# Performance work log

Measured on AMD Instinct MI355X. Metric: run time of the kernel, lower is better.

## Reference

```python
import jax, jax.numpy as jnp
import numpy as np

N_NODES = 10000
N_EDGES = 160000
HID = 256
NBOND = 6
NATOM = 62
NLAYERS = 6


def _lin_init(key, fan_in, fan_out):
    # torch nn.Linear default: U(-1/sqrt(fan_in), 1/sqrt(fan_in))
    kw, kb = jax.random.split(key)
    bound = 1.0 / np.sqrt(fan_in)
    w = jax.random.uniform(kw, (fan_in, fan_out), jnp.float32, -bound, bound)
    b = jax.random.uniform(kb, (fan_out,), jnp.float32, -bound, bound)
    return w, b


def setup_inputs() -> dict:
    key = jax.random.key(0)
    ks = jax.random.split(key, 32)
    atom_features = jax.random.normal(ks[0], (N_NODES, NATOM), jnp.float32)
    edge_index = jax.random.randint(ks[1], (2, N_EDGES), 0, N_NODES, jnp.int64 if jax.config.jax_enable_x64 else jnp.int32)
    edge_features = jax.random.normal(ks[2], (N_EDGES, NBOND), jnp.float32)

    embed_w, embed_b = _lin_init(ks[3], NATOM, HID)

    msg_in = 2 * HID + NBOND  # 518
    mw1, mb1, mw2, mb2 = [], [], [], []
    uw1, ub1, uw2, ub2 = [], [], [], []
    for i in range(NLAYERS):
        k = jax.random.split(ks[4 + i], 4)
        w, b = _lin_init(k[0], msg_in, HID); mw1.append(w); mb1.append(b)
        w, b = _lin_init(k[1], HID, HID); mw2.append(w); mb2.append(b)
        w, b = _lin_init(k[2], 2 * HID, HID); uw1.append(w); ub1.append(b)
        w, b = _lin_init(k[3], HID, HID); uw2.append(w); ub2.append(b)

    r_w1, r_b1 = _lin_init(ks[20], HID, HID)
    r_w2, r_b2 = _lin_init(ks[21], HID, HID // 2)
    r_w3, r_b3 = _lin_init(ks[22], HID // 2, 1)

    return {
        "atom_features": atom_features,
        "edge_index": edge_index,
        "edge_features": edge_features,
        "embed_w": embed_w, "embed_b": embed_b,
        "msg_w1": jnp.stack(mw1), "msg_b1": jnp.stack(mb1),
        "msg_w2": jnp.stack(mw2), "msg_b2": jnp.stack(mb2),
        "upd_w1": jnp.stack(uw1), "upd_b1": jnp.stack(ub1),
        "upd_w2": jnp.stack(uw2), "upd_b2": jnp.stack(ub2),
        "r_w1": r_w1, "r_b1": r_b1,
        "r_w2": r_w2, "r_b2": r_b2,
        "r_w3": r_w3, "r_b3": r_b3,
    }


def _mlp2(x, w1, b1, w2, b2):
    return jnp.maximum(x @ w1 + b1, 0.0) @ w2 + b2


def reference(atom_features, edge_index, edge_features,
              embed_w, embed_b,
              msg_w1, msg_b1, msg_w2, msg_b2,
              upd_w1, upd_b1, upd_w2, upd_b2,
              r_w1, r_b1, r_w2, r_b2, r_w3, r_b3):
    src, dst = edge_index[0], edge_index[1]
    n = atom_features.shape[0]
    x = atom_features @ embed_w + embed_b  # [N, H]
    for l in range(msg_w1.shape[0]):
        # per-edge gather + concat -> message MLP
        msg_in = jnp.concatenate([x[src], x[dst], edge_features], axis=-1)  # [E, 2H+B]
        msgs = _mlp2(msg_in, msg_w1[l], msg_b1[l], msg_w2[l], msg_b2[l])  # [E, H]
        # scatter-add into dst nodes
        agg = jax.ops.segment_sum(msgs, dst, num_segments=n)  # [N, H]
        x = _mlp2(jnp.concatenate([x, agg], axis=-1), upd_w1[l], upd_b1[l], upd_w2[l], upd_b2[l])
    # readout (dropout is identity in eval mode)
    h = jnp.maximum(x @ r_w1 + r_b1, 0.0)
    h = jnp.maximum(h @ r_w2 + r_b2, 0.0)
    out = h @ r_w3 + r_b3  # [N, 1]
    return out.mean(axis=0)  # [1]
```

## Files before the change

### kernel.cpp

```cpp
#include <hip/hip_runtime.h>
#include <hip/hip_bf16.h>
#include <hip/hip_fp16.h>


#define HID 256
#define CAP 128

typedef _Float16 h8 __attribute__((ext_vector_type(8)));
typedef float f32x4 __attribute__((ext_vector_type(4)));

__device__ __forceinline__ void unpack_h8(const int4& r, float* f) {
    const __half2* h = reinterpret_cast<const __half2*>(&r);
#pragma unroll
    for (int k = 0; k < 4; ++k) {
        float2 t = __half22float2(h[k]);
        f[2 * k] = t.x;
        f[2 * k + 1] = t.y;
    }
}

__device__ __forceinline__ void unpack_h4(const int2& r, float* f) {
    const __half2* h = reinterpret_cast<const __half2*>(&r);
    float2 t0 = __half22float2(h[0]);
    float2 t1 = __half22float2(h[1]);
    f[0] = t0.x; f[1] = t0.y; f[2] = t1.x; f[3] = t1.y;
}

__device__ __forceinline__ void gld16(const void* g, void* l) {
    __builtin_amdgcn_global_load_lds(
        (const __attribute__((address_space(1))) void*)g,
        (__attribute__((address_space(3))) void*)l, 16, 0, 0);
}

__device__ __forceinline__ int swz(int row) { return (row + (row >> 2)) & 3; }


struct CDesc {
    const float* src;
    __half* dst;
    int Kreal, Kpad, srcN, tile0, dstStride;
};
struct CTab {
    CDesc d[32];
    int nd;
};

__device__ void convert_body(const CTab& tab, int bid) {
    int idx = 0;
    for (int i = 1; i < tab.nd; ++i)
        if (tab.d[i].tile0 <= bid) idx = i;
    const CDesc d = tab.d[idx];
    const int q = bid - d.tile0;
    const int ntN = d.srcN >> 6;
    const int kb = (q / ntN) * 32;
    const int nb = (q % ntN) * 64;
    const int n = nb + (threadIdx.x & 63);
    const int k0 = kb + (threadIdx.x >> 6) * 8;
    h8 v;
#pragma unroll
    for (int j = 0; j < 8; ++j) {
        int k = k0 + j;
        v[j] = (_Float16)((k < d.Kreal) ? d.src[(size_t)k * d.srcN + n] : 0.f);
    }
    *reinterpret_cast<h8*>(&d.dst[(size_t)n * d.dstStride + k0]) = v;
}


__global__ void conv_kernel(const float* __restrict__ atom,
                            __half* __restrict__ atomH, int NA,
                            int atomB, CTab tab) {
    if ((int)blockIdx.x < atomB) {
        int i = blockIdx.x * blockDim.x + threadIdx.x;
        if (i < NA) {
            int r = i >> 3, seg = i & 7;
            h8 v;
#pragma unroll
            for (int j = 0; j < 8; ++j) {
                int c = seg * 8 + j;
                v[j] = (_Float16)((c < 62) ? atom[(size_t)r * 62 + c] : 0.f);
            }
            *reinterpret_cast<h8*>(&atomH[(size_t)r * 64 + seg * 8]) = v;
        }
    } else {
        convert_body(tab, blockIdx.x - atomB);
    }
}


struct BDesc { float* out; const float* base; const float* v1; const float* B1;
               const float* v2; const float* B2; };
struct BTab { BDesc d[31]; };


#define ASTR 40

struct FDesc { const float* U2; const __half* Wfb; __half* dst; int stride; };
struct FTab { FDesc d[22]; };

__device__ void fold_tile(unsigned char* ldsraw, const FDesc& dd, int t4) {
    _Float16* Ah = (_Float16*)ldsraw;
    _Float16* Bh = (_Float16*)(ldsraw + 64 * ASTR * 2);
    const int rowBase = (t4 >> 2) * 64;
    const int colBase = (t4 & 3) * 64;

    const int tid = threadIdx.x;
    const int lane = tid & 63;
    const int wave = tid >> 6;
    const int waveM = (wave >> 1) * 32;
    const int waveN = (wave & 1) * 32;
    const int m0 = lane & 15;
    const int quad = lane >> 4;
    const int sr = tid >> 2;
    const int sseg = tid & 3;

    const f32x4 z = {0.f, 0.f, 0.f, 0.f};
    f32x4 acc[2][2] = {{z, z}, {z, z}};

    for (int kb = 0; kb < 256; kb += 32) {
        {
            size_t off = (size_t)(rowBase + sr) * 256 + kb + sseg * 8;
            *reinterpret_cast<int4*>(&Ah[sr * ASTR + sseg * 8]) =
                *reinterpret_cast<const int4*>(&dd.Wfb[off]);
        }
        {
            const float* Bp = dd.U2 + (size_t)(colBase + sr) * 256 + kb + sseg * 8;
            float4 u0 = *reinterpret_cast<const float4*>(Bp);
            float4 u1 = *reinterpret_cast<const float4*>(Bp + 4);
            h8 v;
            v[0] = (_Float16)u0.x; v[1] = (_Float16)u0.y;
            v[2] = (_Float16)u0.z; v[3] = (_Float16)u0.w;
            v[4] = (_Float16)u1.x; v[5] = (_Float16)u1.y;
            v[6] = (_Float16)u1.z; v[7] = (_Float16)u1.w;
            *reinterpret_cast<h8*>(&Bh[sr * ASTR + sseg * 8]) = v;
        }
        __syncthreads();

        const h8 a0 = *reinterpret_cast<const h8*>(&Ah[(waveM + m0) * ASTR + quad * 8]);
        const h8 a1 = *reinterpret_cast<const h8*>(&Ah[(waveM + 16 + m0) * ASTR + quad * 8]);
        const h8 b0 = *reinterpret_cast<const h8*>(&Bh[(waveN + m0) * ASTR + quad * 8]);
        const h8 b1 = *reinterpret_cast<const h8*>(&Bh[(waveN + 16 + m0) * ASTR + quad * 8]);

        acc[0][0] = __builtin_amdgcn_mfma_f32_16x16x32_f16(a0, b0, acc[0][0], 0, 0, 0);
        acc[0][1] = __builtin_amdgcn_mfma_f32_16x16x32_f16(a0, b1, acc[0][1], 0, 0, 0);
        acc[1][0] = __builtin_amdgcn_mfma_f32_16x16x32_f16(a1, b0, acc[1][0], 0, 0, 0);
        acc[1][1] = __builtin_amdgcn_mfma_f32_16x16x32_f16(a1, b1, acc[1][1], 0, 0, 0);

        __syncthreads();
    }

#pragma unroll
    for (int tm = 0; tm < 2; ++tm)
#pragma unroll
        for (int reg = 0; reg < 4; ++reg) {
            int n = rowBase + waveM + tm * 16 + quad * 4 + reg;
#pragma unroll
            for (int tn = 0; tn < 2; ++tn) {
                int k = colBase + waveN + tn * 16 + m0;
                dd.dst[(size_t)n * dd.stride + k] = __float2half_rn(acc[tm][tn][reg]);
            }
        }
}


template <int TN>
__device__ void gemm_tile(
    unsigned char* lds, int bx, int by,
    const __half* __restrict__ A, int lda,
    const __half* __restrict__ W, int K,
    const float* __restrict__ bias,
    __half* __restrict__ C, int M, int Nc, int do_relu) {
    constexpr int BUF = 4096 + TN * 2048;

    const int tid = threadIdx.x;
    const int lane = tid & 63;
    const int wave = tid >> 6;
    const int m0 = lane & 15;
    const int quad = lane >> 4;
    const int waveM = (wave >> 1) * 32;
    const int waveN = (wave & 1) * (TN * 16);
    const int rowBase = bx * 64;
    const int colBase = by * (TN * 32);

    const int sa_r = tid >> 2;
    const int sa_ks = (tid & 3) ^ swz(sa_r);
    const int sa_row = min(rowBase + sa_r, M - 1);
    const int sb_r1 = sa_r + 64;
    const int sb_ks1 = (tid & 3) ^ swz(sb_r1);

    int aoff[2], boff[TN];
#pragma unroll
    for (int tm = 0; tm < 2; ++tm) {
        int r = waveM + tm * 16 + m0;
        aoff[tm] = ((r << 2) + (quad ^ swz(r))) << 4;
    }
#pragma unroll
    for (int tn = 0; tn < TN; ++tn) {
        int r = waveN + tn * 16 + m0;
        boff[tn] = 4096 + (((r << 2) + (quad ^ swz(r))) << 4);
    }

    const f32x4 z = {0.f, 0.f, 0.f, 0.f};
    f32x4 acc[2][TN];
#pragma unroll
    for (int tm = 0; tm < 2; ++tm)
#pragma unroll
        for (int tn = 0; tn < TN; ++tn) acc[tm][tn] = z;

    const __half* ga = A + (size_t)sa_row * lda + sa_ks * 8;
    const __half* gb0 = W + (size_t)(colBase + sa_r) * K + sa_ks * 8;
    const __half* gb1 = W + (size_t)(colBase + sb_r1) * K + sb_ks1 * 8;

    auto issue = [&](int p, int kb) {
        unsigned char* base = lds + p * BUF;
        gld16(ga + kb, base + wave * 1024);
        gld16(gb0 + kb, base + 4096 + wave * 1024);
        if constexpr (TN == 4) gld16(gb1 + kb, base + 8192 + wave * 1024);
    };

    issue(0, 0);
    int p = 0;
    for (int kb = 0; kb < K; kb += 32) {
        const bool has_next = (kb + 32 < K);
        if (has_next) issue(p ^ 1, kb + 32);
        if (has_next) {
            if constexpr (TN == 4)
                asm volatile("s_waitcnt vmcnt(3)" ::: "memory");
            else
                asm volatile("s_waitcnt vmcnt(2)" ::: "memory");
        } else {
            asm volatile("s_waitcnt vmcnt(0)" ::: "memory");
        }
        asm volatile("s_barrier" ::: "memory");

        const unsigned char* base = lds + p * BUF;
        h8 ah[2], bh[TN];
#pragma unroll
        for (int tm = 0; tm < 2; ++tm)
            ah[tm] = *reinterpret_cast<const h8*>(base + aoff[tm]);
#pragma unroll
        for (int tn = 0; tn < TN; ++tn)
            bh[tn] = *reinterpret_cast<const h8*>(base + boff[tn]);
#pragma unroll
        for (int tm = 0; tm < 2; ++tm)
#pragma unroll
            for (int tn = 0; tn < TN; ++tn)
                acc[tm][tn] = __builtin_amdgcn_mfma_f32_16x16x32_f16(
                    ah[tm], bh[tn], acc[tm][tn], 0, 0, 0);
        asm volatile("s_waitcnt lgkmcnt(0)" ::: "memory");
        asm volatile("s_barrier" ::: "memory");
        p ^= 1;
    }

    float cb[TN];
    int col[TN];
#pragma unroll
    for (int tn = 0; tn < TN; ++tn) {
        col[tn] = colBase + waveN + tn * 16 + m0;
        cb[tn] = bias ? bias[col[tn]] : 0.f;
    }
#pragma unroll
    for (int tm = 0; tm < 2; ++tm) {
#pragma unroll
        for (int reg = 0; reg < 4; ++reg) {
            int row = rowBase + waveM + tm * 16 + quad * 4 + reg;
            if (row >= M) continue;
#pragma unroll
            for (int tn = 0; tn < TN; ++tn) {
                float v = acc[tm][tn][reg] + cb[tn];
                if (do_relu) v = fmaxf(v, 0.f);
                C[(size_t)row * Nc + col[tn]] = __float2half_rn(v);
            }
        }
    }
}


__global__ __launch_bounds__(256) void scatter_fold_bias_embed_kernel(
    const int* __restrict__ src, const int* __restrict__ dst,
    int* __restrict__ cnt, int* __restrict__ csr_src,
    const float* __restrict__ ef, __half* __restrict__ ef8, int E, int sblocks,
    FTab ft, BTab bt, int fblocks, int bblocks,
    const __half* __restrict__ atomH, const __half* __restrict__ w_emb,
    const float* __restrict__ emb_b, __half* __restrict__ outX,
    int M, int mblk64) {
    __shared__ __align__(16) unsigned char lds[16384];
    int b = blockIdx.x;
    if (b < sblocks) {
        int i = b * 256 + (int)threadIdx.x;
        if (i < E) {
            int d = dst[i];
            int pos = atomicAdd(&cnt[d], 1);
            size_t idx = (size_t)d * CAP + pos;
            csr_src[idx] = src[i];
            const float* s6 = ef + (size_t)i * 6;
            unsigned short h[8];
#pragma unroll
            for (int j = 0; j < 6; ++j) h[j] = __half_as_ushort(__float2half_rn(s6[j]));
            h[6] = 0; h[7] = 0;
            int4 pk;
            pk.x = (int)(h[0] | ((unsigned)h[1] << 16));
            pk.y = (int)(h[2] | ((unsigned)h[3] << 16));
            pk.z = (int)(h[4] | ((unsigned)h[5] << 16));
            pk.w = (int)(h[6] | ((unsigned)h[7] << 16));
            *reinterpret_cast<int4*>(ef8 + idx * 8) = pk;
        }
        return;
    }
    b -= sblocks;
    if (b < fblocks) {
        fold_tile(lds, ft.d[b >> 4], b & 15);
        return;
    }
    b -= fblocks;
    if (b < bblocks) {
        const BDesc d = bt.d[b];
        const int j = threadIdx.x;
        float acc = d.base ? d.base[j] : 0.f;
        if (d.v1)
            for (int k = 0; k < 256; ++k) acc = fmaf(d.v1[k], d.B1[(size_t)k * 256 + j], acc);
        if (d.v2)
            for (int k = 0; k < 256; ++k) acc = fmaf(d.v2[k], d.B2[(size_t)k * 256 + j], acc);
        d.out[j] = acc;
        return;
    }
    b -= bblocks;
    gemm_tile<2>(lds, b % mblk64, b / mblk64, atomH, 64, w_emb, 64,
                 emb_b, outX, M, HID, 0);
}


template <int TN>
__global__ __launch_bounds__(256) void mfma_gemm(
    const __half* __restrict__ A, int lda, const __half* __restrict__ A2,
    const __half* __restrict__ W, int K,
    const float* __restrict__ bias, const float* __restrict__ bias2,
    const float* __restrict__ rowscale,
    __half* __restrict__ C, int M, int Nc, int do_relu) {
    constexpr int BUF = 4096 + TN * 2048;
    __shared__ __align__(16) unsigned char lds[2 * BUF];

    const int tid = threadIdx.x;
    const int lane = tid & 63;
    const int wave = tid >> 6;
    const int m0 = lane & 15;
    const int quad = lane >> 4;
    const int waveM = (wave >> 1) * 32;
    const int waveN = (wave & 1) * (TN * 16);
    const int rowBase = blockIdx.x * 64;
    const int colBase = blockIdx.y * (TN * 32);

    const int sa_r = tid >> 2;
    const int sa_ks = (tid & 3) ^ swz(sa_r);
    const int sa_row = min(rowBase + sa_r, M - 1);
    const int sb_r1 = sa_r + 64;
    const int sb_ks1 = (tid & 3) ^ swz(sb_r1);

    int aoff[2], boff[TN];
#pragma unroll
    for (int tm = 0; tm < 2; ++tm) {
        int r = waveM + tm * 16 + m0;
        aoff[tm] = ((r << 2) + (quad ^ swz(r))) << 4;
    }
#pragma unroll
    for (int tn = 0; tn < TN; ++tn) {
        int r = waveN + tn * 16 + m0;
        boff[tn] = 4096 + (((r << 2) + (quad ^ swz(r))) << 4);
    }

    const f32x4 z = {0.f, 0.f, 0.f, 0.f};
    f32x4 acc[2][TN];
#pragma unroll
    for (int tm = 0; tm < 2; ++tm)
#pragma unroll
        for (int tn = 0; tn < TN; ++tn) acc[tm][tn] = z;

    const __half* ga = A + (size_t)sa_row * lda + sa_ks * 8;
    const __half* ga2 = A2 ? A2 + (size_t)sa_row * lda + sa_ks * 8 : nullptr;
    const __half* gb0 = W + (size_t)(colBase + sa_r) * K + sa_ks * 8;
    const __half* gb1 = W + (size_t)(colBase + sb_r1) * K + sb_ks1 * 8;

    auto issue = [&](int p, int kb) {
        unsigned char* base = lds + p * BUF;
        const __half* as = (A2 && kb >= 256) ? (ga2 + (kb - 256)) : (ga + kb);
        gld16(as, base + wave * 1024);
        gld16(gb0 + kb, base + 4096 + wave * 1024);
        if constexpr (TN == 4) gld16(gb1 + kb, base + 8192 + wave * 1024);
    };

    issue(0, 0);
    int p = 0;
    for (int kb = 0; kb < K; kb += 32) {
        const bool has_next = (kb + 32 < K);
        if (has_next) issue(p ^ 1, kb + 32);
        if (has_next) {
            if constexpr (TN == 4)
                asm volatile("s_waitcnt vmcnt(3)" ::: "memory");
            else
                asm volatile("s_waitcnt vmcnt(2)" ::: "memory");
        } else {
            asm volatile("s_waitcnt vmcnt(0)" ::: "memory");
        }
        asm volatile("s_barrier" ::: "memory");

        const unsigned char* base = lds + p * BUF;
        h8 ah[2], bh[TN];
#pragma unroll
        for (int tm = 0; tm < 2; ++tm)
            ah[tm] = *reinterpret_cast<const h8*>(base + aoff[tm]);
#pragma unroll
        for (int tn = 0; tn < TN; ++tn)
            bh[tn] = *reinterpret_cast<const h8*>(base + boff[tn]);
#pragma unroll
        for (int tm = 0; tm < 2; ++tm)
#pragma unroll
            for (int tn = 0; tn < TN; ++tn)
                acc[tm][tn] = __builtin_amdgcn_mfma_f32_16x16x32_f16(
                    ah[tm], bh[tn], acc[tm][tn], 0, 0, 0);
        asm volatile("s_waitcnt lgkmcnt(0)" ::: "memory");
        asm volatile("s_barrier" ::: "memory");
        p ^= 1;
    }

    float cb[TN], db[TN];
    int col[TN];
#pragma unroll
    for (int tn = 0; tn < TN; ++tn) {
        col[tn] = colBase + waveN + tn * 16 + m0;
        cb[tn] = bias ? bias[col[tn]] : 0.f;
        db[tn] = bias2 ? bias2[col[tn]] : 0.f;
    }
#pragma unroll
    for (int tm = 0; tm < 2; ++tm) {
#pragma unroll
        for (int reg = 0; reg < 4; ++reg) {
            int row = rowBase + waveM + tm * 16 + quad * 4 + reg;
            if (row >= M) continue;
            float rs = rowscale ? rowscale[row] : 0.0f;
#pragma unroll
            for (int tn = 0; tn < TN; ++tn) {
                float v = acc[tm][tn][reg] + cb[tn] + rs * db[tn];
                if (do_relu) v = fmaxf(v, 0.f);
                C[(size_t)row * Nc + col[tn]] = __float2half_rn(v);
            }
        }
    }
}


__global__ __launch_bounds__(256) void aggregate_kernel(
    const __half* __restrict__ PQ, const __half* __restrict__ ef8,
    const int* __restrict__ cnt, const int* __restrict__ csr_src,
    const float* __restrict__ W1c, __half* __restrict__ Hagg,
    float* __restrict__ degf_out, int n) {
    const int wave = threadIdx.x >> 6;
    const int lane = threadIdx.x & 63;
    const int node = blockIdx.x * 4 + wave;
    if (node >= n) return;
    const int ch = lane * 4;

    float wc[6][4];
#pragma unroll
    for (int k = 0; k < 6; ++k) {
        float4 w0 = *reinterpret_cast<const float4*>(W1c + k * HID + ch);
        wc[k][0] = w0.x; wc[k][1] = w0.y; wc[k][2] = w0.z; wc[k][3] = w0.w;
    }
    float qb[4];
    unpack_h4(*reinterpret_cast<const int2*>(PQ + (size_t)node * 512 + 256 + ch), qb);

    float acc[4] = {0.f, 0.f, 0.f, 0.f};

    auto fma_edge = [&](const int2& praw, const int4& eraw) {
        float p[4], e[8];
        unpack_h4(praw, p);
        unpack_h8(eraw, e);
#pragma unroll
        for (int i = 0; i < 4; ++i) {
            float h = p[i] + qb[i];
            h = fmaf(e[0], wc[0][i], h);
            h = fmaf(e[1], wc[1][i], h);
            h = fmaf(e[2], wc[2][i], h);
            h = fmaf(e[3], wc[3][i], h);
            h = fmaf(e[4], wc[4][i], h);
            h = fmaf(e[5], wc[5][i], h);
            acc[i] += fmaxf(h, 0.f);
        }
    };

    const int beg = node * CAP;
    const int deg = cnt[node];
    const int end = beg + deg;
    if (degf_out && lane == 0) degf_out[node] = (float)deg;
    int j = beg;

    while (j + 6 <= end) {
        int s0 = csr_src[j];
        int s1 = csr_src[j + 1];
        int s2 = csr_src[j + 2];
        int s3 = csr_src[j + 3];
        int s4 = csr_src[j + 4];
        int s5 = csr_src[j + 5];
        int4 e0 = *reinterpret_cast<const int4*>(ef8 + (size_t)j * 8);
        int4 e1 = *reinterpret_cast<const int4*>(ef8 + (size_t)(j + 1) * 8);
        int4 e2 = *reinterpret_cast<const int4*>(ef8 + (size_t)(j + 2) * 8);
        int4 e3 = *reinterpret_cast<const int4*>(ef8 + (size_t)(j + 3) * 8);
        int4 e4 = *reinterpret_cast<const int4*>(ef8 + (size_t)(j + 4) * 8);
        int4 e5 = *reinterpret_cast<const int4*>(ef8 + (size_t)(j + 5) * 8);
        int2 p0 = *reinterpret_cast<const int2*>(PQ + (size_t)s0 * 512 + ch);
        int2 p1 = *reinterpret_cast<const int2*>(PQ + (size_t)s1 * 512 + ch);
        int2 p2 = *reinterpret_cast<const int2*>(PQ + (size_t)s2 * 512 + ch);
        int2 p3 = *reinterpret_cast<const int2*>(PQ + (size_t)s3 * 512 + ch);
        int2 p4 = *reinterpret_cast<const int2*>(PQ + (size_t)s4 * 512 + ch);
        int2 p5 = *reinterpret_cast<const int2*>(PQ + (size_t)s5 * 512 + ch);
        fma_edge(p0, e0);
        fma_edge(p1, e1);
        fma_edge(p2, e2);
        fma_edge(p3, e3);
        fma_edge(p4, e4);
        fma_edge(p5, e5);
        j += 6;
    }
    while (j + 2 <= end) {
        int s0 = csr_src[j];
        int s1 = csr_src[j + 1];
        int4 e0 = *reinterpret_cast<const int4*>(ef8 + (size_t)j * 8);
        int4 e1 = *reinterpret_cast<const int4*>(ef8 + (size_t)(j + 1) * 8);
        int2 p0 = *reinterpret_cast<const int2*>(PQ + (size_t)s0 * 512 + ch);
        int2 p1 = *reinterpret_cast<const int2*>(PQ + (size_t)s1 * 512 + ch);
        fma_edge(p0, e0);
        fma_edge(p1, e1);
        j += 2;
    }
    if (j < end) {
        int s = csr_src[j];
        int4 e = *reinterpret_cast<const int4*>(ef8 + (size_t)j * 8);
        int2 pw = *reinterpret_cast<const int2*>(PQ + (size_t)s * 512 + ch);
        fma_edge(pw, e);
    }

    unsigned short hs[4];
#pragma unroll
    for (int i = 0; i < 4; ++i) hs[i] = __half_as_ushort(__float2half_rn(acc[i]));
    int2 pk;
    pk.x = (int)(hs[0] | ((unsigned)hs[1] << 16));
    pk.y = (int)(hs[2] | ((unsigned)hs[3] << 16));
    *reinterpret_cast<int2*>(Hagg + (size_t)node * HID + ch) = pk;
}


__global__ __launch_bounds__(256) void readout_kernel(
    const __half* __restrict__ U5, const __half* __restrict__ wF,
    const float* __restrict__ cbF, const __half* __restrict__ wR2,
    const float* __restrict__ bR2, const float* __restrict__ w3,
    const float* __restrict__ b3, float* __restrict__ accum,
    int* __restrict__ done, float* __restrict__ outp, int M, int nblocks) {
    __shared__ __align__(16) unsigned char lds[24576 + 64 * 272 * 2];
    _Float16* h1 = (_Float16*)(lds + 24576);

    const int tid = threadIdx.x;
    const int lane = tid & 63;
    const int wave = tid >> 6;
    const int m0 = lane & 15;
    const int quad = lane >> 4;
    const int waveM = (wave >> 1) * 32;
    const int waveN = (wave & 1) * 64;
    const int rowBase = blockIdx.x * 64;

    const int sa_r = tid >> 2;
    const int sa_ks = (tid & 3) ^ swz(sa_r);
    const int sa_row = min(rowBase + sa_r, M - 1);
    const int sb_r1 = sa_r + 64;
    const int sb_ks1 = (tid & 3) ^ swz(sb_r1);

    int aoff[2], boff[4];
#pragma unroll
    for (int tm = 0; tm < 2; ++tm) {
        int r = waveM + tm * 16 + m0;
        aoff[tm] = ((r << 2) + (quad ^ swz(r))) << 4;
    }
#pragma unroll
    for (int tn = 0; tn < 4; ++tn) {
        int r = waveN + tn * 16 + m0;
        boff[tn] = (((r << 2) + (quad ^ swz(r))) << 4);
    }

    constexpr int BUF = 4096 + 4 * 2048;
    const f32x4 z = {0.f, 0.f, 0.f, 0.f};

    for (int half = 0; half < 2; ++half) {
        const __half* W = wF + (size_t)(half * 128) * 256;
        f32x4 acc[2][4] = {{z, z, z, z}, {z, z, z, z}};
        const __half* ga = U5 + (size_t)sa_row * 256 + sa_ks * 8;
        const __half* gb0 = W + (size_t)sa_r * 256 + sa_ks * 8;
        const __half* gb1 = W + (size_t)sb_r1 * 256 + sb_ks1 * 8;

        auto issue = [&](int p, int kb) {
            unsigned char* base = lds + p * BUF;
            gld16(ga + kb, base + wave * 1024);
            gld16(gb0 + kb, base + 4096 + wave * 1024);
            gld16(gb1 + kb, base + 8192 + wave * 1024);
        };
        issue(0, 0);
        int p = 0;
        for (int kb = 0; kb < 256; kb += 32) {
            const bool has_next = (kb + 32 < 256);
            if (has_next) issue(p ^ 1, kb + 32);
            if (has_next) asm volatile("s_waitcnt vmcnt(3)" ::: "memory");
            else asm volatile("s_waitcnt vmcnt(0)" ::: "memory");
            asm volatile("s_barrier" ::: "memory");
            const unsigned char* base = lds + p * BUF;
            h8 ah[2], bh[4];
#pragma unroll
            for (int tm = 0; tm < 2; ++tm)
                ah[tm] = *reinterpret_cast<const h8*>(base + aoff[tm]);
#pragma unroll
            for (int tn = 0; tn < 4; ++tn)
                bh[tn] = *reinterpret_cast<const h8*>(base + 4096 + boff[tn]);
#pragma unroll
            for (int tm = 0; tm < 2; ++tm)
#pragma unroll
                for (int tn = 0; tn < 4; ++tn)
                    acc[tm][tn] = __builtin_amdgcn_mfma_f32_16x16x32_f16(
                        ah[tm], bh[tn], acc[tm][tn], 0, 0, 0);
            asm volatile("s_waitcnt lgkmcnt(0)" ::: "memory");
            asm volatile("s_barrier" ::: "memory");
            p ^= 1;
        }
#pragma unroll
        for (int tm = 0; tm < 2; ++tm)
#pragma unroll
            for (int reg = 0; reg < 4; ++reg) {
                int r = waveM + tm * 16 + quad * 4 + reg;
#pragma unroll
                for (int tn = 0; tn < 4; ++tn) {
                    int c = half * 128 + waveN + tn * 16 + m0;
                    float v = acc[tm][tn][reg] + cbF[c];
                    h1[r * 272 + c] = (_Float16)fmaxf(v, 0.f);
                }
            }
        __syncthreads();
    }

    f32x4 acc2[2][4] = {{z, z, z, z}, {z, z, z, z}};
    auto issueB = [&](int p, int kb) {
        unsigned char* base = lds + p * 8192;
        gld16(wR2 + (size_t)sa_r * 256 + sa_ks * 8 + kb, base + wave * 1024);
        gld16(wR2 + (size_t)sb_r1 * 256 + sb_ks1 * 8 + kb, base + 4096 + wave * 1024);
    };
    issueB(0, 0);
    int p = 0;
    for (int kb = 0; kb < 256; kb += 32) {
        const bool has_next = (kb + 32 < 256);
        if (has_next) issueB(p ^ 1, kb + 32);
        if (has_next) asm volatile("s_waitcnt vmcnt(2)" ::: "memory");
        else asm volatile("s_waitcnt vmcnt(0)" ::: "memory");
        asm volatile("s_barrier" ::: "memory");
        const unsigned char* base = lds + p * 8192;
        h8 ah[2], bh[4];
#pragma unroll
        for (int tm = 0; tm < 2; ++tm)
            ah[tm] = *reinterpret_cast<const h8*>(
                &h1[(waveM + tm * 16 + m0) * 272 + kb + quad * 8]);
#pragma unroll
        for (int tn = 0; tn < 4; ++tn)
            bh[tn] = *reinterpret_cast<const h8*>(base + boff[tn]);
#pragma unroll
        for (int tm = 0; tm < 2; ++tm)
#pragma unroll
            for (int tn = 0; tn < 4; ++tn)
                acc2[tm][tn] = __builtin_amdgcn_mfma_f32_16x16x32_f16(
                    ah[tm], bh[tn], acc2[tm][tn], 0, 0, 0);
        asm volatile("s_waitcnt lgkmcnt(0)" ::: "memory");
        asm volatile("s_barrier" ::: "memory");
        p ^= 1;
    }

    float s = 0.f;
#pragma unroll
    for (int tm = 0; tm < 2; ++tm)
#pragma unroll
        for (int reg = 0; reg < 4; ++reg) {
            int row = rowBase + waveM + tm * 16 + quad * 4 + reg;
            if (row >= M) continue;
#pragma unroll
            for (int tn = 0; tn < 4; ++tn) {
                int c = waveN + tn * 16 + m0;
                float v = acc2[tm][tn][reg] + bR2[c];
                s += fmaxf(v, 0.f) * w3[c];
            }
        }
    __syncthreads();
    float* red = (float*)lds;
    red[tid] = s;
    __syncthreads();
    for (int off = 128; off > 0; off >>= 1) {
        if (tid < off) red[tid] += red[tid + off];
        __syncthreads();
    }
    if (tid == 0) {
        atomicAdd(accum, red[0]);
        __threadfence();
        int old = atomicAdd(done, 1);
        if (old == nblocks - 1) {
            float tot = atomicAdd(accum, 0.0f);
            outp[0] = tot / (float)M + b3[0];
        }
    }
}


extern "C" void kernel_launch(void* const* d_in, const int* in_sizes, int n_in,
                              void* d_out, int out_size, void* d_ws, size_t ws_size,
                              hipStream_t stream) {
    const float* atom   = (const float*)d_in[0];
    const int*   eidx   = (const int*)d_in[1];
    const float* ef     = (const float*)d_in[2];
    const float* emb_w  = (const float*)d_in[3];
    const float* emb_b  = (const float*)d_in[4];
    const float* msg_w1 = (const float*)d_in[5];
    const float* msg_b1 = (const float*)d_in[6];
    const float* msg_w2 = (const float*)d_in[7];
    const float* msg_b2 = (const float*)d_in[8];
    const float* upd_w1 = (const float*)d_in[9];
    const float* upd_b1 = (const float*)d_in[10];
    const float* upd_w2 = (const float*)d_in[11];
    const float* upd_b2 = (const float*)d_in[12];
    const float* r_w1   = (const float*)d_in[13];
    const float* r_b1   = (const float*)d_in[14];
    const float* r_w2   = (const float*)d_in[15];
    const float* r_b2   = (const float*)d_in[16];
    const float* r_w3   = (const float*)d_in[17];
    const float* r_b3   = (const float*)d_in[18];

    const int N = in_sizes[0] / 62;
    const int E = in_sizes[1] / 2;
    const int L = in_sizes[5] / (518 * 256);
    const int* src = eidx;
    const int* dst = eidx + E;

    char* wp = (char*)d_ws;
    auto alloc = [&](size_t bytes) -> void* {
        void* p = (void*)wp;
        wp += (bytes + 255) & ~(size_t)255;
        return p;
    };
    int*   cnt     = (int*)alloc((size_t)N * 4);
    float* accum   = (float*)alloc(256);
    int*   done    = (int*)((char*)accum + 16);
    size_t zero_bytes = (size_t)((char*)accum - (char*)d_ws) + 256;
    float* degf    = (float*)alloc((size_t)N * 4);
    int*   csr_src = (int*)alloc((size_t)N * CAP * 4);
    __half* ef8    = (__half*)alloc((size_t)N * CAP * 8 * 2);

    const int SQ_P = 256 * 256;
    __half* w_emb = (__half*)alloc((size_t)256 * 64 * 2);
    __half* w_r2  = (__half*)alloc((size_t)128 * 256 * 2);
    __half* wF    = (__half*)alloc((size_t)SQ_P * 2);
    __half *wPQ[6], *wUPD[6];
    for (int l = 0; l < L; ++l) {
        wPQ[l]  = (__half*)alloc((size_t)512 * 256 * 2);
        wUPD[l] = (__half*)alloc((size_t)256 * 512 * 2);
    }
    __half* fb[22];
    for (int i = 0; i < 22; ++i) fb[i] = (__half*)alloc((size_t)SQ_P * 2);
    float* bvec = (float*)alloc((size_t)19 * 256 * 4);
    float* b512 = (float*)alloc((size_t)L * 512 * 4);

    __half* atomH = (__half*)alloc((size_t)N * 64 * 2);
    __half* bufX0 = (__half*)alloc((size_t)N * HID * 2);
    __half* bufX1 = (__half*)alloc((size_t)N * HID * 2);
    __half* PQ    = (__half*)alloc((size_t)N * 512 * 2);
    __half* HaggH = (__half*)alloc((size_t)N * HID * 2);

    hipMemsetAsync(d_ws, 0, zero_bytes, stream);

    CTab ct1;
    int nd = 0, tiles = 0;
    auto addDesc = [&](const float* s, __half* dh, int Kreal, int Kpad, int srcN,
                       int dstStride) {
        ct1.d[nd] = {s, dh, Kreal, Kpad, srcN, tiles, dstStride};
        tiles += (Kpad / 32) * (srcN / 64);
        ++nd;
    };
    addDesc(emb_w, w_emb, 62, 64, 256, 64);
    addDesc(msg_w1, wPQ[0], 256, 256, 256, 256);
    addDesc(msg_w1 + 256 * 256, wPQ[0] + SQ_P, 256, 256, 256, 256);
    addDesc(upd_w1, wUPD[0] + 256, 256, 256, 256, 512);
    addDesc(r_w2, w_r2, 256, 256, 128, 256);
    for (int l = 1; l < L; ++l) {
        addDesc(msg_w1 + (size_t)l * 518 * 256,             fb[l - 1], 256, 256, 256, 256);
        addDesc(msg_w1 + (size_t)l * 518 * 256 + 256 * 256, fb[4 + l], 256, 256, 256, 256);
        addDesc(upd_w1 + (size_t)l * 512 * 256,             fb[9 + l], 256, 256, 256, 256);
    }
    for (int l = 0; l < L; ++l)
        addDesc(upd_w1 + (size_t)l * 512 * 256 + 256 * 256, fb[15 + l], 256, 256, 256, 256);
    addDesc(r_w1, fb[21], 256, 256, 256, 256);
    ct1.nd = nd;

    const int atomB = (N * 8 + 255) / 256;
    conv_kernel<<<atomB + tiles, 256, 0, stream>>>(atom, atomH, N * 8, atomB, ct1);

    FTab ft;
    for (int l = 1; l < L; ++l) {
        const float* U2p = upd_w2 + (size_t)(l - 1) * SQ_P;
        ft.d[l - 1] = {U2p, fb[l - 1], wPQ[l], 256};
        ft.d[4 + l] = {U2p, fb[4 + l], wPQ[l] + SQ_P, 256};
        ft.d[9 + l] = {U2p, fb[9 + l], wUPD[l] + 256, 512};
    }
    for (int l = 0; l < L; ++l)
        ft.d[15 + l] = {msg_w2 + (size_t)l * SQ_P, fb[15 + l], wUPD[l], 512};
    ft.d[21] = {upd_w2 + (size_t)5 * SQ_P, fb[21], wF, 256};

    BTab bt;
    int nb = 0;
    for (int l = 0; l < L; ++l) {
        const float* ub2p = (l > 0) ? upd_b2 + (size_t)(l - 1) * 256 : nullptr;
        bt.d[nb++] = {b512 + (size_t)l * 512 + 256, msg_b1 + (size_t)l * 256,
                      ub2p, msg_w1 + (size_t)l * 518 * 256,
                      ub2p, msg_w1 + (size_t)l * 518 * 256 + 256 * 256};
        bt.d[nb++] = {b512 + (size_t)l * 512, nullptr, nullptr, nullptr, nullptr, nullptr};
        bt.d[nb++] = {bvec + (size_t)(6 + l) * 256, upd_b1 + (size_t)l * 256,
                      ub2p, upd_w1 + (size_t)l * 512 * 256, nullptr, nullptr};
        bt.d[nb++] = {bvec + (size_t)(12 + l) * 256, nullptr,
                      msg_b2 + (size_t)l * 256, upd_w1 + (size_t)l * 512 * 256 + 256 * 256,
                      nullptr, nullptr};
    }
    bt.d[nb++] = {bvec + (size_t)18 * 256, r_b1, upd_b2 + (size_t)5 * 256, r_w1,
                  nullptr, nullptr};

    const int sblocks = (E + 255) / 256;
    const int fblocks = 22 * 16;
    const int mblk64 = (N + 63) / 64;
    scatter_fold_bias_embed_kernel<<<sblocks + fblocks + nb + mblk64 * 4, 256, 0,
                                     stream>>>(
        src, dst, cnt, csr_src, ef, ef8, E, sblocks,
        ft, bt, fblocks, nb, atomH, w_emb, emb_b, bufX0, N, mblk64);

    dim3 blk(256);
    __half* U_prev = bufX0;
    __half* U_next = bufX1;
    for (int l = 0; l < L; ++l) {
        const float* w1c = msg_w1 + (size_t)l * 518 * 256 + 512 * 256;

        mfma_gemm<4><<<dim3(mblk64, 4), blk, 0, stream>>>(
            U_prev, HID, nullptr, wPQ[l], HID,
            b512 + (size_t)l * 512, nullptr, nullptr,
            PQ, N, 512, 0);
        aggregate_kernel<<<(N + 3) / 4, blk, 0, stream>>>(
            PQ, ef8, cnt, csr_src, w1c, HaggH, (l == 0) ? degf : nullptr, N);
        mfma_gemm<2><<<dim3(mblk64, 4), blk, 0, stream>>>(
            HaggH, HID, U_prev, wUPD[l], 512,
            bvec + (size_t)(6 + l) * 256, bvec + (size_t)(12 + l) * 256, degf,
            U_next, N, 256, 1);
        __half* t = U_prev; U_prev = U_next; U_next = t;
    }

    readout_kernel<<<mblk64, blk, 0, stream>>>(
        U_prev, wF, bvec + (size_t)18 * 256, w_r2, r_b2, r_w3, r_b3,
        accum, done, (float*)d_out, N, mblk64);
}
```

Baseline: 408.3 us.

## Fold conversion kernel into setup kernel; read fp32 weights directly in fold and embed

Removes the separate conversion kernel launch. The fold tiles now read fp32 source weights directly with strided loads and convert them in registers, so the intermediate fp16 transposed buffers are gone. The embedding GEMM reads the fp32 atom features and embedding weights directly, and the remaining weight conversions run as extra blocks in the single setup kernel. This saves a launch and an intermediate round trip through memory, at the cost of uncoalesced strided fp32 reads in the fold and embed tiles.

```diff
diff --git a/kernel.cpp b/kernel.cpp
--- a/kernel.cpp
+++ b/kernel.cpp
@@ -41,7 +41,7 @@
     int Kreal, Kpad, srcN, tile0, dstStride;
 };
 struct CTab {
-    CDesc d[32];
+    CDesc d[8];
     int nd;
 };
 
@@ -66,27 +66,6 @@
 }
 
 
-__global__ void conv_kernel(const float* __restrict__ atom,
-                            __half* __restrict__ atomH, int NA,
-                            int atomB, CTab tab) {
-    if ((int)blockIdx.x < atomB) {
-        int i = blockIdx.x * blockDim.x + threadIdx.x;
-        if (i < NA) {
-            int r = i >> 3, seg = i & 7;
-            h8 v;
-#pragma unroll
-            for (int j = 0; j < 8; ++j) {
-                int c = seg * 8 + j;
-                v[j] = (_Float16)((c < 62) ? atom[(size_t)r * 62 + c] : 0.f);
-            }
-            *reinterpret_cast<h8*>(&atomH[(size_t)r * 64 + seg * 8]) = v;
-        }
-    } else {
-        convert_body(tab, blockIdx.x - atomB);
-    }
-}
-
-
 struct BDesc { float* out; const float* base; const float* v1; const float* B1;
                const float* v2; const float* B2; };
 struct BTab { BDesc d[31]; };
@@ -94,7 +73,7 @@
 
 #define ASTR 40
 
-struct FDesc { const float* U2; const __half* Wfb; __half* dst; int stride; };
+struct FDesc { const float* U2; const float* srcA; __half* dst; int stride; };
 struct FTab { FDesc d[22]; };
 
 __device__ void fold_tile(unsigned char* ldsraw, const FDesc& dd, int t4) {
@@ -118,9 +97,11 @@
 
     for (int kb = 0; kb < 256; kb += 32) {
         {
-            size_t off = (size_t)(rowBase + sr) * 256 + kb + sseg * 8;
-            *reinterpret_cast<int4*>(&Ah[sr * ASTR + sseg * 8]) =
-                *reinterpret_cast<const int4*>(&dd.Wfb[off]);
+            const float* Ap = dd.srcA + (size_t)(kb + sseg * 8) * 256 + rowBase + sr;
+            h8 v;
+#pragma unroll
+            for (int j = 0; j < 8; ++j) v[j] = (_Float16)Ap[(size_t)j * 256];
+            *reinterpret_cast<h8*>(&Ah[sr * ASTR + sseg * 8]) = v;
         }
         {
             const float* Bp = dd.U2 + (size_t)(colBase + sr) * 256 + kb + sseg * 8;
@@ -162,125 +143,86 @@
 }
 
 
-template <int TN>
-__device__ void gemm_tile(
-    unsigned char* lds, int bx, int by,
-    const __half* __restrict__ A, int lda,
-    const __half* __restrict__ W, int K,
-    const float* __restrict__ bias,
-    __half* __restrict__ C, int M, int Nc, int do_relu) {
-    constexpr int BUF = 4096 + TN * 2048;
+__device__ void embed_tile(unsigned char* ldsraw, int bx, int by,
+                           const float* __restrict__ atom,
+                           const float* __restrict__ emb_w,
+                           const float* __restrict__ emb_b,
+                           __half* __restrict__ outX, int M) {
+    _Float16* Ah = (_Float16*)ldsraw;
+    _Float16* Bh = (_Float16*)(ldsraw + 64 * ASTR * 2);
+    const int rowBase = bx * 64;
+    const int colBase = by * 64;
 
     const int tid = threadIdx.x;
     const int lane = tid & 63;
     const int wave = tid >> 6;
+    const int waveM = (wave >> 1) * 32;
+    const int waveN = (wave & 1) * 32;
     const int m0 = lane & 15;
     const int quad = lane >> 4;
-    const int waveM = (wave >> 1) * 32;
-    const int waveN = (wave & 1) * (TN * 16);
-    const int rowBase = bx * 64;
-    const int colBase = by * (TN * 32);
-
-    const int sa_r = tid >> 2;
-    const int sa_ks = (tid & 3) ^ swz(sa_r);
-    const int sa_row = min(rowBase + sa_r, M - 1);
-    const int sb_r1 = sa_r + 64;
-    const int sb_ks1 = (tid & 3) ^ swz(sb_r1);
-
-    int aoff[2], boff[TN];
-#pragma unroll
-    for (int tm = 0; tm < 2; ++tm) {
-        int r = waveM + tm * 16 + m0;
-        aoff[tm] = ((r << 2) + (quad ^ swz(r))) << 4;
-    }
-#pragma unroll
-    for (int tn = 0; tn < TN; ++tn) {
-        int r = waveN + tn * 16 + m0;
-        boff[tn] = 4096 + (((r << 2) + (quad ^ swz(r))) << 4);
-    }
+    const int sr = tid >> 2;
+    const int sseg = tid & 3;
 
     const f32x4 z = {0.f, 0.f, 0.f, 0.f};
-    f32x4 acc[2][TN];
+    f32x4 acc[2][2] = {{z, z}, {z, z}};
+
+    for (int kb = 0; kb < 64; kb += 32) {
+        {
+            const int arow = min(rowBase + sr, M - 1);
+            h8 v;
+#pragma unroll
+            for (int j = 0; j < 8; ++j) {
+                int k = kb + sseg * 8 + j;
+                v[j] = (_Float16)((k < 62) ? atom[(size_t)arow * 62 + k] : 0.f);
+            }
+            *reinterpret_cast<h8*>(&Ah[sr * ASTR + sseg * 8]) = v;
+        }
+        {
+            h8 v;
+#pragma unroll
+            for (int j = 0; j < 8; ++j) {
+                int k = kb + sseg * 8 + j;
+                v[j] = (_Float16)((k < 62) ? emb_w[(size_t)k * 256 + colBase + sr] : 0.f);
+            }
+            *reinterpret_cast<h8*>(&Bh[sr * ASTR + sseg * 8]) = v;
+        }
+        __syncthreads();
+
+        const h8 a0 = *reinterpret_cast<const h8*>(&Ah[(waveM + m0) * ASTR + quad * 8]);
+        const h8 a1 = *reinterpret_cast<const h8*>(&Ah[(waveM + 16 + m0) * ASTR + quad * 8]);
+        const h8 b0 = *reinterpret_cast<const h8*>(&Bh[(waveN + m0) * ASTR + quad * 8]);
+        const h8 b1 = *reinterpret_cast<const h8*>(&Bh[(waveN + 16 + m0) * ASTR + quad * 8]);
+
+        acc[0][0] = __builtin_amdgcn_mfma_f32_16x16x32_f16(a0, b0, acc[0][0], 0, 0, 0);
+        acc[0][1] = __builtin_amdgcn_mfma_f32_16x16x32_f16(a0, b1, acc[0][1], 0, 0, 0);
+        acc[1][0] = __builtin_amdgcn_mfma_f32_16x16x32_f16(a1, b0, acc[1][0], 0, 0, 0);
+        acc[1][1] = __builtin_amdgcn_mfma_f32_16x16x32_f16(a1, b1, acc[1][1], 0, 0, 0);
+
+        __syncthreads();
+    }
+
 #pragma unroll
     for (int tm = 0; tm < 2; ++tm)
-#pragma unroll
-        for (int tn = 0; tn < TN; ++tn) acc[tm][tn] = z;
-
-    const __half* ga = A + (size_t)sa_row * lda + sa_ks * 8;
-    const __half* gb0 = W + (size_t)(colBase + sa_r) * K + sa_ks * 8;
-    const __half* gb1 = W + (size_t)(colBase + sb_r1) * K + sb_ks1 * 8;
-
-    auto issue = [&](int p, int kb) {
-        unsigned char* base = lds + p * BUF;
-        gld16(ga + kb, base + wave * 1024);
-        gld16(gb0 + kb, base + 4096 + wave * 1024);
-        if constexpr (TN == 4) gld16(gb1 + kb, base + 8192 + wave * 1024);
-    };
-
-    issue(0, 0);
-    int p = 0;
-    for (int kb = 0; kb < K; kb += 32) {
-        const bool has_next = (kb + 32 < K);
-        if (has_next) issue(p ^ 1, kb + 32);
-        if (has_next) {
-            if constexpr (TN == 4)
-                asm volatile("s_waitcnt vmcnt(3)" ::: "memory");
-            else
-                asm volatile("s_waitcnt vmcnt(2)" ::: "memory");
-        } else {
-            asm volatile("s_waitcnt vmcnt(0)" ::: "memory");
-        }
-        asm volatile("s_barrier" ::: "memory");
-
-        const unsigned char* base = lds + p * BUF;
-        h8 ah[2], bh[TN];
-#pragma unroll
-        for (int tm = 0; tm < 2; ++tm)
-            ah[tm] = *reinterpret_cast<const h8*>(base + aoff[tm]);
-#pragma unroll
-        for (int tn = 0; tn < TN; ++tn)
-            bh[tn] = *reinterpret_cast<const h8*>(base + boff[tn]);
-#pragma unroll
-        for (int tm = 0; tm < 2; ++tm)
-#pragma unroll
-            for (int tn = 0; tn < TN; ++tn)
-                acc[tm][tn] = __builtin_amdgcn_mfma_f32_16x16x32_f16(
-                    ah[tm], bh[tn], acc[tm][tn], 0, 0, 0);
-        asm volatile("s_waitcnt lgkmcnt(0)" ::: "memory");
-        asm volatile("s_barrier" ::: "memory");
-        p ^= 1;
-    }
-
-    float cb[TN];
-    int col[TN];
-#pragma unroll
-    for (int tn = 0; tn < TN; ++tn) {
-        col[tn] = colBase + waveN + tn * 16 + m0;
-        cb[tn] = bias ? bias[col[tn]] : 0.f;
-    }
-#pragma unroll
-    for (int tm = 0; tm < 2; ++tm) {
 #pragma unroll
         for (int reg = 0; reg < 4; ++reg) {
             int row = rowBase + waveM + tm * 16 + quad * 4 + reg;
             if (row >= M) continue;
 #pragma unroll
-            for (int tn = 0; tn < TN; ++tn) {
-                float v = acc[tm][tn][reg] + cb[tn];
-                if (do_relu) v = fmaxf(v, 0.f);
-                C[(size_t)row * Nc + col[tn]] = __float2half_rn(v);
+            for (int tn = 0; tn < 2; ++tn) {
+                int col = colBase + waveN + tn * 16 + m0;
+                outX[(size_t)row * 256 + col] =
+                    __float2half_rn(acc[tm][tn][reg] + emb_b[col]);
             }
         }
-    }
-}
-
-
-__global__ __launch_bounds__(256) void scatter_fold_bias_embed_kernel(
+}
+
+
+__global__ __launch_bounds__(256) void setup_kernel(
     const int* __restrict__ src, const int* __restrict__ dst,
     int* __restrict__ cnt, int* __restrict__ csr_src,
     const float* __restrict__ ef, __half* __restrict__ ef8, int E, int sblocks,
-    FTab ft, BTab bt, int fblocks, int bblocks,
-    const __half* __restrict__ atomH, const __half* __restrict__ w_emb,
+    FTab ft, BTab bt, int fblocks, int bblocks, CTab ct, int cblocks,
+    const float* __restrict__ atom, const float* __restrict__ emb_w,
     const float* __restrict__ emb_b, __half* __restrict__ outX,
     int M, int mblk64) {
     __shared__ __align__(16) unsigned char lds[16384];
@@ -324,8 +266,12 @@
         return;
     }
     b -= bblocks;
-    gemm_tile<2>(lds, b % mblk64, b / mblk64, atomH, 64, w_emb, 64,
-                 emb_b, outX, M, HID, 0);
+    if (b < cblocks) {
+        convert_body(ct, b);
+        return;
+    }
+    b -= cblocks;
+    embed_tile(lds, b % mblk64, b / mblk64, atom, emb_w, emb_b, outX, M);
 }
 
 
@@ -752,7 +698,6 @@
     __half* ef8    = (__half*)alloc((size_t)N * CAP * 8 * 2);
 
     const int SQ_P = 256 * 256;
-    __half* w_emb = (__half*)alloc((size_t)256 * 64 * 2);
     __half* w_r2  = (__half*)alloc((size_t)128 * 256 * 2);
     __half* wF    = (__half*)alloc((size_t)SQ_P * 2);
     __half *wPQ[6], *wUPD[6];
@@ -760,12 +705,9 @@
         wPQ[l]  = (__half*)alloc((size_t)512 * 256 * 2);
         wUPD[l] = (__half*)alloc((size_t)256 * 512 * 2);
     }
-    __half* fb[22];
-    for (int i = 0; i < 22; ++i) fb[i] = (__half*)alloc((size_t)SQ_P * 2);
     float* bvec = (float*)alloc((size_t)19 * 256 * 4);
     float* b512 = (float*)alloc((size_t)L * 512 * 4);
 
-    __half* atomH = (__half*)alloc((size_t)N * 64 * 2);
     __half* bufX0 = (__half*)alloc((size_t)N * HID * 2);
     __half* bufX1 = (__half*)alloc((size_t)N * HID * 2);
     __half* PQ    = (__half*)alloc((size_t)N * 512 * 2);
@@ -773,42 +715,32 @@
 
     hipMemsetAsync(d_ws, 0, zero_bytes, stream);
 
-    CTab ct1;
-    int nd = 0, tiles = 0;
+    CTab ct;
+    int nd = 0, ctiles = 0;
     auto addDesc = [&](const float* s, __half* dh, int Kreal, int Kpad, int srcN,
                        int dstStride) {
-        ct1.d[nd] = {s, dh, Kreal, Kpad, srcN, tiles, dstStride};
-        tiles += (Kpad / 32) * (srcN / 64);
+        ct.d[nd] = {s, dh, Kreal, Kpad, srcN, ctiles, dstStride};
+        ctiles += (Kpad / 32) * (srcN / 64);
         ++nd;
     };
-    addDesc(emb_w, w_emb, 62, 64, 256, 64);
     addDesc(msg_w1, wPQ[0], 256, 256, 256, 256);
     addDesc(msg_w1 + 256 * 256, wPQ[0] + SQ_P, 256, 256, 256, 256);
     addDesc(upd_w1, wUPD[0] + 256, 256, 256, 256, 512);
     addDesc(r_w2, w_r2, 256, 256, 128, 256);
-    for (int l = 1; l < L; ++l) {
-        addDesc(msg_w1 + (size_t)l * 518 * 256,             fb[l - 1], 256, 256, 256, 256);
-        addDesc(msg_w1 + (size_t)l * 518 * 256 + 256 * 256, fb[4 + l], 256, 256, 256, 256);
-        addDesc(upd_w1 + (size_t)l * 512 * 256,             fb[9 + l], 256, 256, 256, 256);
-    }
-    for (int l = 0; l < L; ++l)
-        addDesc(upd_w1 + (size_t)l * 512 * 256 + 256 * 256, fb[15 + l], 256, 256, 256, 256);
-    addDesc(r_w1, fb[21], 256, 256, 256, 256);
-    ct1.nd = nd;
-
-    const int atomB = (N * 8 + 255) / 256;
-    conv_kernel<<<atomB + tiles, 256, 0, stream>>>(atom, atomH, N * 8, atomB, ct1);
+    ct.nd = nd;
 
     FTab ft;
     for (int l = 1; l < L; ++l) {
         const float* U2p = upd_w2 + (size_t)(l - 1) * SQ_P;
-        ft.d[l - 1] = {U2p, fb[l - 1], wPQ[l], 256};
-        ft.d[4 + l] = {U2p, fb[4 + l], wPQ[l] + SQ_P, 256};
-        ft.d[9 + l] = {U2p, fb[9 + l], wUPD[l] + 256, 512};
+        ft.d[l - 1] = {U2p, msg_w1 + (size_t)l * 518 * 256, wPQ[l], 256};
+        ft.d[4 + l] = {U2p, msg_w1 + (size_t)l * 518 * 256 + 256 * 256,
+                       wPQ[l] + SQ_P, 256};
+        ft.d[9 + l] = {U2p, upd_w1 + (size_t)l * 512 * 256, wUPD[l] + 256, 512};
     }
     for (int l = 0; l < L; ++l)
-        ft.d[15 + l] = {msg_w2 + (size_t)l * SQ_P, fb[15 + l], wUPD[l], 512};
-    ft.d[21] = {upd_w2 + (size_t)5 * SQ_P, fb[21], wF, 256};
+        ft.d[15 + l] = {msg_w2 + (size_t)l * SQ_P,
+                        upd_w1 + (size_t)l * 512 * 256 + 256 * 256, wUPD[l], 512};
+    ft.d[21] = {upd_w2 + (size_t)5 * SQ_P, r_w1, wF, 256};
 
     BTab bt;
     int nb = 0;
@@ -830,10 +762,11 @@
     const int sblocks = (E + 255) / 256;
     const int fblocks = 22 * 16;
     const int mblk64 = (N + 63) / 64;
-    scatter_fold_bias_embed_kernel<<<sblocks + fblocks + nb + mblk64 * 4, 256, 0,
-                                     stream>>>(
+    const int grid2 = sblocks + fblocks + nb + ctiles + mblk64 * 4;
+    setup_kernel<<<grid2, 256, 0, stream>>>(
         src, dst, cnt, csr_src, ef, ef8, E, sblocks,
-        ft, bt, fblocks, nb, atomH, w_emb, emb_b, bufX0, N, mblk64);
+        ft, bt, fblocks, nb, ct, ctiles,
+        atom, emb_w, emb_b, bufX0, N, mblk64);
 
     dim3 blk(256);
     __half* U_prev = bufX0;
```

New measurement: 399.2 us (median of 2 runs). 2.2% less time.
